# Optimization experiments

Measured on AMD Instinct MI355X. Metric: run time of the kernel, lower is better.

The kernel has to match this reference:

```python
import jax, jax.numpy as jnp
import numpy as np

STRIDES = (8, 16, 32)
SIZES = ((80, 80), (40, 40), (20, 20))  # 640x640 input
PRE_TOP_K = 1000
KEEP_TOP_K = 100
IOU_THR = 0.65
SCORE_THR = 0.25
CLASS_OFFSET = 4096.0  # > max image extent, for class-aware NMS


def setup_inputs() -> dict:
    key = jax.random.key(0)
    ks = jax.random.split(key, 6)
    B, C = 8, 1203
    d = {}
    for i, (h, w) in enumerate(SIZES):
        d[f"cls_scores_{i}"] = jax.random.normal(ks[i], (B, C, h, w), dtype=jnp.float32)
        d[f"bbox_preds_{i}"] = jax.random.uniform(ks[3 + i], (B, 4, h, w), dtype=jnp.float32)
    return d


def _flatten(feats, ch):
    B = feats[0].shape[0]
    return jnp.concatenate([f.transpose(0, 2, 3, 1).reshape(B, -1, ch) for f in feats], axis=1)


def _priors():
    pts, strs = [], []
    for (h, w), s in zip(SIZES, STRIDES):
        yy, xx = jnp.meshgrid(jnp.arange(h, dtype=jnp.float32), jnp.arange(w, dtype=jnp.float32), indexing="ij")
        pts.append(jnp.stack([(xx.ravel() + 0.5) * s, (yy.ravel() + 0.5) * s], axis=-1))
        strs.append(jnp.full((h * w,), float(s), dtype=jnp.float32))
    return jnp.concatenate(pts, 0), jnp.concatenate(strs, 0)


def _decode(priors, preds, stride):
    # DistancePointBBoxCoder: preds are LTRB distances scaled by stride.
    d = preds * stride[None, :, None]  # [B,N,4]
    x1 = priors[None, :, 0] - d[..., 0]
    y1 = priors[None, :, 1] - d[..., 1]
    x2 = priors[None, :, 0] + d[..., 2]
    y2 = priors[None, :, 1] + d[..., 3]
    return jnp.stack([x1, y1, x2, y2], axis=-1)


def _iou_matrix(b):
    area = (b[:, 2] - b[:, 0]) * (b[:, 3] - b[:, 1])
    lt = jnp.maximum(b[:, None, :2], b[None, :, :2])
    rb = jnp.minimum(b[:, None, 2:], b[None, :, 2:])
    wh = jnp.clip(rb - lt, 0.0)
    inter = wh[..., 0] * wh[..., 1]
    return inter / (area[:, None] + area[None, :] - inter + 1e-7)


def _nms_single(boxes, scores, labels):
    # boxes [N,4], scores [N] (max over classes), labels [N] int
    ts, idx = jax.lax.top_k(scores, PRE_TOP_K)
    b = boxes[idx]
    l = labels[idx]
    valid = ts > SCORE_THR
    off = b + (l.astype(b.dtype) * CLASS_OFFSET)[:, None]  # class-aware trick
    iou = _iou_matrix(off)  # [K,K]

    def body(keep, i):
        suppressed = jnp.any(keep & (iou[:, i] > IOU_THR))
        keep = keep.at[i].set(valid[i] & ~suppressed)
        return keep, None

    keep, _ = jax.lax.scan(body, jnp.zeros((PRE_TOP_K,), bool), jnp.arange(PRE_TOP_K))
    kept_scores = jnp.where(keep, ts, -1.0)
    fs, fi = jax.lax.top_k(kept_scores, KEEP_TOP_K)
    m = fs > 0.0
    det_boxes = jnp.where(m[:, None], b[fi], 0.0)
    det_scores = jnp.where(m, fs, 0.0)
    det_labels = jnp.where(m, l[fi], -1)
    num_dets = m.sum().astype(jnp.int32)
    return num_dets, det_boxes, det_scores, det_labels


def reference(cls_scores_0, cls_scores_1, cls_scores_2, bbox_preds_0, bbox_preds_1, bbox_preds_2):
    C = cls_scores_0.shape[1]
    cls_scores = jax.nn.sigmoid(_flatten([cls_scores_0, cls_scores_1, cls_scores_2], C))  # [B,N,C]
    preds = _flatten([bbox_preds_0, bbox_preds_1, bbox_preds_2], 4)  # [B,N,4]
    priors, stride = _priors()
    boxes = _decode(priors, preds, stride)  # [B,N,4]
    max_scores = cls_scores.max(axis=-1)  # [B,N]
    labels = cls_scores.argmax(axis=-1)  # [B,N]
    num_dets, det_boxes, det_scores, det_labels = jax.vmap(_nms_single)(boxes, max_scores, labels)
    return num_dets, det_boxes, det_scores, det_labels
```

## Files before the change

### kernel.cpp

```cpp
#include <hip/hip_runtime.h>
#include <math.h>

#pragma clang fp contract(off)

typedef unsigned long long u64;
typedef unsigned int u32;
typedef float f4 __attribute__((ext_vector_type(4)));
typedef unsigned long long u64x2 __attribute__((ext_vector_type(2)));

#define BB 8
#define CC_TOT 1203
#define NANC 8400
#define NSEL 1000
#define NCAND 1024
#define NT 1024
#define NBATCH 128
#define NCHUNK_MAX 16

__device__ __forceinline__ u32 okey32(float v) {
  u32 b = __float_as_uint(v);
  return (b & 0x80000000u) ? ~b : (b | 0x80000000u);
}

__device__ __forceinline__ float unokey32(u32 ok) {
  u32 fb = (ok & 0x80000000u) ? (ok & 0x7FFFFFFFu) : ~ok;
  return __uint_as_float(fb);
}

__global__ __launch_bounds__(256) void kmax(const float* __restrict__ cls0,
                                            const float* __restrict__ cls1,
                                            const float* __restrict__ cls2,
                                            u64* __restrict__ part,
                                            int chunkSz, int nchunk) {
  int bx = blockIdx.x;
  int per = nchunk * BB;
  int tg = bx / per;
  int rem = bx - tg * per;
  int chunk = rem >> 3;
  int b = rem & 7;
  const float* cls; int hw4, aoff, col0;
  if (tg < 7)      { cls = cls0; hw4 = 1600; aoff = 0;    col0 = tg << 8; }
  else if (tg < 9) { cls = cls1; hw4 = 400;  aoff = 6400; col0 = (tg - 7) << 8; }
  else             { cls = cls2; hw4 = 100;  aoff = 8000; col0 = 0; }
  int col = col0 + (int)threadIdx.x;
  if (col >= hw4) return;
  int c0 = chunk * chunkSz;
  int c1 = c0 + chunkSz; if (c1 > CC_TOT) c1 = CC_TOT;

  const f4* base = (const f4*)cls + (size_t)b * CC_TOT * hw4 + col;
  f4 m = (f4){-3.4e38f, -3.4e38f, -3.4e38f, -3.4e38f};
  int ix0 = c0, ix1 = c0, ix2 = c0, ix3 = c0;

#define UPD(v, c)                                   \
  do {                                              \
    if ((v)[0] > m[0]) { m[0] = (v)[0]; ix0 = (c); } \
    if ((v)[1] > m[1]) { m[1] = (v)[1]; ix1 = (c); } \
    if ((v)[2] > m[2]) { m[2] = (v)[2]; ix2 = (c); } \
    if ((v)[3] > m[3]) { m[3] = (v)[3]; ix3 = (c); } \
  } while (0)

  int c = c0;
  for (; c + 8 <= c1; c += 8) {
    const f4* p = base + (size_t)c * hw4;
    f4 v0 = p[0];
    f4 v1 = p[(size_t)1 * hw4];
    f4 v2 = p[(size_t)2 * hw4];
    f4 v3 = p[(size_t)3 * hw4];
    f4 v4 = p[(size_t)4 * hw4];
    f4 v5 = p[(size_t)5 * hw4];
    f4 v6 = p[(size_t)6 * hw4];
    f4 v7 = p[(size_t)7 * hw4];
    UPD(v0, c + 0); UPD(v1, c + 1); UPD(v2, c + 2); UPD(v3, c + 3);
    UPD(v4, c + 4); UPD(v5, c + 5); UPD(v6, c + 6); UPD(v7, c + 7);
  }
  for (; c < c1; ++c) {
    f4 v = base[(size_t)c * hw4];
    UPD(v, c);
  }
#undef UPD

  u64* dst = part + ((size_t)chunk * BB + b) * NANC + aoff + (size_t)col * 4;
  u64x2 s01 = { ((u64)okey32(m[0]) << 32) | (u64)(u32)~(u32)ix0,
                ((u64)okey32(m[1]) << 32) | (u64)(u32)~(u32)ix1 };
  u64x2 s23 = { ((u64)okey32(m[2]) << 32) | (u64)(u32)~(u32)ix2,
                ((u64)okey32(m[3]) << 32) | (u64)(u32)~(u32)ix3 };
  *((u64x2*)dst)     = s01;
  *((u64x2*)dst + 1) = s23;
}

struct DecodeArrays {
  float xo1[NCAND], yo1[NCAND], xo2[NCAND], yo2[NCAND], ar[NCAND];
  float rx1[NCAND], ry1[NCAND], rx2[NCAND], ry2[NCAND], sc[NCAND];
  int lab[NCAND], val[NCAND];
};

__device__ __forceinline__ u64x2 reduce_pair(const u64x2* psrc, size_t PL2, int nchunk, int i) {
  u64x2 m = psrc[i];
  for (int ch = 1; ch < nchunk; ++ch) {
    u64x2 v = psrc[(size_t)ch * PL2 + i];
    if (v[0] > m[0]) m[0] = v[0];
    if (v[1] > m[1]) m[1] = v[1];
  }
  u32 i0 = (u32)(2 * i), i1 = (u32)(2 * i + 1);
  u64x2 r;
  r[0] = (m[0] & 0xFFFFFFFF00000000ull) | ((u64)(0xFFFFu - i0) << 16) | (u64)(~(u32)m[0] & 0xFFFFu);
  r[1] = (m[1] & 0xFFFFFFFF00000000ull) | ((u64)(0xFFFFu - i1) << 16) | (u64)(~(u32)m[1] & 0xFFFFu);
  return r;
}

__device__ __forceinline__ void hist_add12(u32* hist, u32 digit, int lane) {
  u64 peers = ~0ull;
  for (int bit = 0; bit < 12; ++bit) {
    u64 bal = __ballot((digit >> bit) & 1u);
    peers &= ((digit >> bit) & 1u) ? bal : ~bal;
  }
  int leader = __ffsll((unsigned long long)peers) - 1;
  if (lane == leader)
    atomicAdd(&hist[digit], (u32)__popcll((unsigned long long)peers));
}

__device__ __forceinline__ void hist_add_clustered(u32* hist, u32 digit, int lane) {
  u64 peers = ~0ull;
  for (int bit = 0; bit < 13; ++bit) {
    u64 bal = __ballot((digit >> bit) & 1u);
    peers &= ((digit >> bit) & 1u) ? bal : ~bal;
  }
  int leader = __ffsll((unsigned long long)peers) - 1;
  if (digit < 4096u && lane == leader)
    atomicAdd(&hist[digit], (u32)__popcll((unsigned long long)peers));
}

__device__ __forceinline__ void suffix_pick(u32* hist, u32* waveTot, u32* waveSufExcl,
                                            u64* prefixSh, u32* rankSh, u32* binCntSh,
                                            u64 prefix, u32 rank, int shift,
                                            int tid, int lane, int wv) {
  u32 l0 = hist[4 * tid], l1 = hist[4 * tid + 1], l2 = hist[4 * tid + 2], l3 = hist[4 * tid + 3];
  u32 psum = l0 + l1 + l2 + l3;
  u32 x = psum;
  for (int s = 1; s < 64; s <<= 1) { u32 v = __shfl_down(x, s); if (lane + s < 64) x += v; }
  if (lane == 0) waveTot[wv] = x;
  __syncthreads();
  if (tid < 16) {
    u32 y = waveTot[tid]; u32 z = y;
    for (int s = 1; s < 16; s <<= 1) { u32 v = __shfl_down(z, s); if (tid + s < 16) z += v; }
    waveSufExcl[tid] = z - y;
  }
  __syncthreads();
  u32 S = x + waveSufExcl[wv];
  u32 G3 = S - psum; u32 G2 = G3 + l3; u32 G1 = G2 + l2; u32 G0 = G1 + l1;
  u32 r = rank;
  if      (G3 < r && G3 + l3 >= r) { *prefixSh = prefix | ((u64)(4u * tid + 3) << shift); *rankSh = r - G3; *binCntSh = l3; }
  else if (G2 < r && G2 + l2 >= r) { *prefixSh = prefix | ((u64)(4u * tid + 2) << shift); *rankSh = r - G2; *binCntSh = l2; }
  else if (G1 < r && G1 + l1 >= r) { *prefixSh = prefix | ((u64)(4u * tid + 1) << shift); *rankSh = r - G1; *binCntSh = l1; }
  else if (G0 < r && G0 + l0 >= r) { *prefixSh = prefix | ((u64)(4u * tid + 0) << shift); *rankSh = r - G0; *binCntSh = l0; }
}

__device__ __forceinline__ u64 radix_select(const u64* keys, int n, u32 target,
                                            u32* hist, u32* waveTot, u32* waveSufExcl,
                                            u64* prefixSh, u32* rankSh, u32* binCntSh,
                                            int tid, int lane, int wv) {
  u64 prefix = 0; u32 rank = target;
  for (int pass = 3; pass >= 0; --pass) {
    int shift = 16 + pass * 12;
    for (int i = tid; i < 4096; i += NT) hist[i] = 0;
    __syncthreads();
    u64 hiMask = (pass == 3) ? 0ull : ((~0ull) << (shift + 12));
    if (pass == 3) {
      for (int i = tid; i < n; i += NT) {
        u64 k = keys[i];
        hist_add_clustered(hist, (u32)((k >> shift) & 4095u), lane);
      }
    } else {
      for (int i = tid; i < n; i += NT) {
        u64 k = keys[i];
        if ((k & hiMask) == (prefix & hiMask))
          atomicAdd(&hist[(u32)((k >> shift) & 4095u)], 1u);
      }
    }
    __syncthreads();
    suffix_pick(hist, waveTot, waveSufExcl, prefixSh, rankSh, binCntSh, prefix, rank, shift, tid, lane, wv);
    __syncthreads();
    prefix = *prefixSh; rank = *rankSh;
    __syncthreads();
  }
  return prefix;
}

__device__ __forceinline__ void gather_ge(const u64* keys, int n, u64 K, u64* dst, u32* cnt,
                                          int tid, int lane, u32 bound) {
  for (int i = tid; i < n; i += NT) {
    u64 k = keys[i];
    bool sel = (k >= K);
    u64 mask = __ballot(sel);
    if (mask) {
      int leader = __ffsll((unsigned long long)mask) - 1;
      u32 basep = 0;
      if (lane == leader) basep = atomicAdd(cnt, (u32)__popcll((unsigned long long)mask));
      basep = __shfl((int)basep, leader);
      if (sel) {
        u32 pos = basep + (u32)__popcll((unsigned long long)(mask & ((1ull << lane) - 1ull)));
        if (pos < bound) dst[pos] = k;
      }
    }
  }
}

__device__ __forceinline__ void decode_into(DecodeArrays* d, int rk, u64 my, int b,
                                            const float* bb0, const float* bb1, const float* bb2) {
  int label = (int)(u32)(my & 0xFFFFull);
  int idx = 0xFFFF - (int)(u32)((my >> 16) & 0xFFFFull);
  float logit = unokey32((u32)(my >> 32));
  float sc = 1.0f / (1.0f + expf(-logit));

  int w, str, off, hwl; const float* bb;
  if (idx < 6400)      { w = 80; str = 8;  off = 0;    hwl = 6400; bb = bb0; }
  else if (idx < 8000) { w = 40; str = 16; off = 6400; hwl = 1600; bb = bb1; }
  else                 { w = 20; str = 32; off = 8000; hwl = 400;  bb = bb2; }
  int p = idx - off;
  int y = p / w;
  int x = p - y * w;
  float fs = (float)str;
  float px = ((float)x + 0.5f) * fs;
  float py = ((float)y + 0.5f) * fs;
  const float* bp = bb + (size_t)b * 4 * hwl + p;
  float t0 = bp[0] * fs;
  float t1 = bp[hwl] * fs;
  float t2 = bp[2 * hwl] * fs;
  float t3 = bp[3 * hwl] * fs;
  float x1 = px - t0, y1 = py - t1, x2 = px + t2, y2 = py + t3;
  float lo = (float)label * 4096.0f;
  float ox1 = x1 + lo, oy1 = y1 + lo, ox2 = x2 + lo, oy2 = y2 + lo;
  float area = (ox2 - ox1) * (oy2 - oy1);

  d->xo1[rk] = ox1; d->yo1[rk] = oy1; d->xo2[rk] = ox2; d->yo2[rk] = oy2; d->ar[rk] = area;
  d->rx1[rk] = x1;  d->ry1[rk] = y1;  d->rx2[rk] = x2;  d->ry2[rk] = y2;  d->sc[rk] = sc;
  d->lab[rk] = label;
  d->val[rk] = (sc > 0.25f) ? 1 : 0;
}

__device__ __forceinline__ int nms_pass(const DecodeArrays* d, int bound, int lane, int* outIdx) {
  float ax1 = 0, ay1 = 0, ax2 = 0, ay2 = 0, aar = 0; int aon = 0;
  float bx1 = 0, by1 = 0, bx2 = 0, by2 = 0, bar = 0; int bon = 0;
  int kept = 0;
  for (int i = 0; i < bound; ++i) {
    if (kept >= 100) break;
    float cx1 = d->xo1[i], cy1 = d->yo1[i], cx2 = d->xo2[i], cy2 = d->yo2[i], car = d->ar[i];
    bool sup = false;
    if (aon) {
      float ltx = fmaxf(ax1, cx1), lty = fmaxf(ay1, cy1);
      float rbx = fminf(ax2, cx2), rby = fminf(ay2, cy2);
      float wd = fmaxf(rbx - ltx, 0.0f), ht = fmaxf(rby - lty, 0.0f);
      float inter = wd * ht;
      sup = sup || ((inter / (aar + car - inter + 1e-7f)) > 0.65f);
    }
    if (bon) {
      float ltx = fmaxf(bx1, cx1), lty = fmaxf(by1, cy1);
      float rbx = fminf(bx2, cx2), rby = fminf(by2, cy2);
      float wd = fmaxf(rbx - ltx, 0.0f), ht = fmaxf(rby - lty, 0.0f);
      float inter = wd * ht;
      sup = sup || ((inter / (bar + car - inter + 1e-7f)) > 0.65f);
    }
    bool anysup = __any(sup);
    if (d->val[i] != 0 && !anysup) {
      if (kept < 64) {
        if (lane == kept) { ax1 = cx1; ay1 = cy1; ax2 = cx2; ay2 = cy2; aar = car; aon = 1; }
      } else {
        if (lane == kept - 64) { bx1 = cx1; by1 = cy1; bx2 = cx2; by2 = cy2; bar = car; bon = 1; }
      }
      if (lane == 0) outIdx[kept] = i;
      ++kept;
    }
  }
  return kept;
}

__global__ __launch_bounds__(1024) void knms(const u64* __restrict__ part, int nchunk,
                                             const float* __restrict__ bb0,
                                             const float* __restrict__ bb1,
                                             const float* __restrict__ bb2,
                                             float* __restrict__ out) {
  __shared__ union ShU {
    u64 fk[NANC];
    DecodeArrays d;
  } sh;
  __shared__ u32 hist[4096];
  __shared__ u32 waveTot[16];
  __shared__ u32 waveSufExcl[16];
  __shared__ u64 prefixSh;
  __shared__ u32 rankSh, binCntSh;
  __shared__ u32 gcnt, aCnt, cCnt;
  __shared__ __align__(16) u64 cand[NCAND];
  __shared__ __align__(16) u64 candA[NBATCH];
  __shared__ __align__(16) u32 cm[NBATCH * 4];
  __shared__ u64 VwSh[2];
  __shared__ int outIdx[128];
  __shared__ int keptSh;

  int b = blockIdx.x;
  int tid = threadIdx.x;
  int lane = tid & 63;
  int wv = tid >> 6;

  const u64x2* psrc = (const u64x2*)(part + (size_t)b * NANC);
  const size_t PL2 = (size_t)BB * NANC / 2;

  for (int i = tid; i < 4096; i += NT) hist[i] = 0;
  if (tid == 0) { aCnt = 0; cCnt = 0; }
  __syncthreads();
  {
    u64x2* fdst = (u64x2*)sh.fk;
    for (int i = tid; i < NANC / 2; i += NT) {
      u64x2 k = reduce_pair(psrc, PL2, nchunk, i);
      fdst[i] = k;
      hist_add12(hist, (u32)(k[0] >> 52), lane);
      hist_add12(hist, (u32)(k[1] >> 52), lane);
    }
  }
  __syncthreads();

  suffix_pick(hist, waveTot, waveSufExcl, &prefixSh, &rankSh, &binCntSh,
              0ull, NBATCH, 52, tid, lane, wv);
  __syncthreads();
  u64 pfx3 = prefixSh; u32 r3 = rankSh; u32 l3 = binCntSh;
  u32 d3 = (u32)(pfx3 >> 52);
  __syncthreads();

  bool pathological = false;
  if (l3 == r3) {
    gather_ge(sh.fk, NANC, pfx3, candA, &aCnt, tid, lane, NBATCH);
    __syncthreads();
  } else {
    for (int i = tid; i < NANC; i += NT) {
      u64 k = sh.fk[i];
      u32 dig = (u32)(k >> 52);
      bool selA = dig > d3;
      u64 mA = __ballot(selA);
      if (mA) {
        int leader = __ffsll((unsigned long long)mA) - 1;
        u32 basep = 0;
        if (lane == leader) basep = atomicAdd(&aCnt, (u32)__popcll((unsigned long long)mA));
        basep = __shfl((int)basep, leader);
        if (selA) {
          u32 pos = basep + (u32)__popcll((unsigned long long)(mA & ((1ull << lane) - 1ull)));
          if (pos < NBATCH) candA[pos] = k;
        }
      }
      bool selC = (dig == d3);
      u64 mC = __ballot(selC);
      if (mC) {
        int leader = __ffsll((unsigned long long)mC) - 1;
        u32 basep = 0;
        if (lane == leader) basep = atomicAdd(&cCnt, (u32)__popcll((unsigned long long)mC));
        basep = __shfl((int)basep, leader);
        if (selC) {
          u32 pos = basep + (u32)__popcll((unsigned long long)(mC & ((1ull << lane) - 1ull)));
          if (pos < NCAND) cand[pos] = k;
        }
      }
    }
    __syncthreads();

    u32 cnt3 = cCnt;
    if (cnt3 <= NCAND) {
      u64 pfx = pfx3; u32 rk = r3;
      u64 Kf = 0; bool done = false;
      for (int pass = 2; pass >= 0 && !done; --pass) {
        int shift = 16 + pass * 12;
        for (int i = tid; i < 4096; i += NT) hist[i] = 0;
        __syncthreads();
        u64 hiMask = (~0ull) << (shift + 12);
        for (int i = tid; i < (int)cnt3; i += NT) {
          u64 k = cand[i];
          if ((k & hiMask) == (pfx & hiMask))
            atomicAdd(&hist[(u32)((k >> shift) & 4095u)], 1u);
        }
        __syncthreads();
        suffix_pick(hist, waveTot, waveSufExcl, &prefixSh, &rankSh, &binCntSh,
                    pfx, rk, shift, tid, lane, wv);
        __syncthreads();
        pfx = prefixSh; rk = rankSh;
        u32 lc = binCntSh;
        __syncthreads();
        if (lc == rk || pass == 0) { done = true; Kf = pfx; }
      }
      gather_ge(cand, (int)cnt3, Kf, candA, &aCnt, tid, lane, NBATCH);
      __syncthreads();
    } else {
      pathological = true;
    }
  }

  if (pathological) {
    if (tid == 0) aCnt = 0;
    __syncthreads();
    u64 K2 = radix_select(sh.fk, NANC, NBATCH, hist, waveTot, waveSufExcl,
                          &prefixSh, &rankSh, &binCntSh, tid, lane, wv);
    gather_ge(sh.fk, NANC, K2, candA, &aCnt, tid, lane, NBATCH);
    __syncthreads();
  }

  if (tid < NBATCH) {
    u64 my = candA[tid];
    int rk = 0;
    const u64x2* cav = (const u64x2*)candA;
    #pragma unroll
    for (int j2 = 0; j2 < NBATCH / 2; ++j2) {
      u64x2 p = cav[j2];
      rk += (p[0] > my) ? 1 : 0;
      rk += (p[1] > my) ? 1 : 0;
    }
    decode_into(&sh.d, rk, my, b, bb0, bb1, bb2);
  }
  if (tid < NBATCH * 4) cm[tid] = 0;
  __syncthreads();

  if (tid < NBATCH) {
    u64 bal = __ballot(sh.d.val[tid] != 0);
    if (lane == 0) VwSh[tid >> 6] = bal;
  }

  {
    int c = tid & 127;
    int g = tid >> 7;
    float cx1 = sh.d.xo1[c], cy1 = sh.d.yo1[c], cx2 = sh.d.xo2[c], cy2 = sh.d.yo2[c], car = sh.d.ar[c];
    u32 bits = 0;
    int j0 = g * 16;
    for (int jj = 0; jj < 16; ++jj) {
      int j = j0 + jj;
      float ltx = fmaxf(sh.d.xo1[j], cx1), lty = fmaxf(sh.d.yo1[j], cy1);
      float rbx = fminf(sh.d.xo2[j], cx2), rby = fminf(sh.d.yo2[j], cy2);
      float wd = fmaxf(rbx - ltx, 0.0f), ht = fmaxf(rby - lty, 0.0f);
      float inter = wd * ht;
      bool sup = (inter / (sh.d.ar[j] + car - inter + 1e-7f)) > 0.65f;
      bits |= sup ? (1u << jj) : 0u;
    }
    atomicOr(&cm[c * 4 + (g >> 1)], bits << ((g & 1) * 16));
  }
  __syncthreads();

  if (tid == 0) {
    u32 L0 = (u32)VwSh[0], L1 = (u32)(VwSh[0] >> 32);
    u32 L2 = (u32)VwSh[1], L3 = (u32)(VwSh[1] >> 32);
    int kept = 0;
    while (kept < 100) {
      int i;
      if (L0)      i = __ffs(L0) - 1;
      else if (L1) i = 31 + __ffs(L1);
      else if (L2) i = 63 + __ffs(L2);
      else if (L3) i = 95 + __ffs(L3);
      else break;
      outIdx[kept++] = i;
      const u32* c4 = &cm[i * 4];
      L0 &= ~c4[0]; L1 &= ~c4[1]; L2 &= ~c4[2]; L3 &= ~c4[3];
      if (i < 32)      L0 &= ~(1u << i);
      else if (i < 64) L1 &= ~(1u << (i - 32));
      else if (i < 96) L2 &= ~(1u << (i - 64));
      else             L3 &= ~(1u << (i - 96));
    }
    keptSh = kept;
  }
  __syncthreads();

  if (keptSh < 100) {
    {
      u64x2* fdst = (u64x2*)sh.fk;
      for (int i = tid; i < NANC / 2; i += NT)
        fdst[i] = reduce_pair(psrc, PL2, nchunk, i);
    }
    __syncthreads();
    u64 K = radix_select(sh.fk, NANC, NSEL, hist, waveTot, waveSufExcl,
                         &prefixSh, &rankSh, &binCntSh, tid, lane, wv);
    if (tid == 0) gcnt = 0;
    __syncthreads();
    gather_ge(sh.fk, NANC, K, cand, &gcnt, tid, lane, NSEL);
    __syncthreads();
    if (tid < NSEL) {
      u64 my = cand[tid];
      int rk = 0;
      const u64x2* cbv = (const u64x2*)cand;
      for (int j2 = 0; j2 < NSEL / 2; ++j2) {
        u64x2 p = cbv[j2];
        rk += (p[0] > my) ? 1 : 0;
        rk += (p[1] > my) ? 1 : 0;
      }
      decode_into(&sh.d, rk, my, b, bb0, bb1, bb2);
    }
    __syncthreads();
    if (tid < 64) {
      int kept = nms_pass(&sh.d, NSEL, lane, outIdx);
      if (lane == 0) keptSh = kept;
    }
    __syncthreads();
  }

  int kept = keptSh;
  float* o_nd = out;
  float* o_box = out + BB;
  float* o_sc = out + BB + BB * 100 * 4;
  float* o_lb = out + BB + BB * 100 * 4 + BB * 100;
  if (tid == 0) o_nd[b] = (float)kept;
  if (tid < 100) {
    int s = tid;
    float v0 = 0, v1 = 0, v2 = 0, v3 = 0, sv = 0, lv = -1.0f;
    if (s < kept) {
      int i = outIdx[s];
      v0 = sh.d.rx1[i]; v1 = sh.d.ry1[i]; v2 = sh.d.rx2[i]; v3 = sh.d.ry2[i];
      sv = sh.d.sc[i]; lv = (float)sh.d.lab[i];
    }
    float* bo = o_box + ((size_t)b * 100 + s) * 4;
    bo[0] = v0; bo[1] = v1; bo[2] = v2; bo[3] = v3;
    o_sc[b * 100 + s] = sv;
    o_lb[b * 100 + s] = lv;
  }
}

extern "C" void kernel_launch(void* const* d_in, const int* in_sizes, int n_in,
                              void* d_out, int out_size, void* d_ws, size_t ws_size,
                              hipStream_t stream) {
  const float* cls0 = (const float*)d_in[0];
  const float* bb0  = (const float*)d_in[1];
  const float* cls1 = (const float*)d_in[2];
  const float* bb1  = (const float*)d_in[3];
  const float* cls2 = (const float*)d_in[4];
  const float* bb2  = (const float*)d_in[5];

  size_t planeB = (size_t)BB * NANC * sizeof(u64);
  u64* part = (u64*)d_ws;
  int nchunk = (int)(ws_size / planeB);
  if (nchunk < 1) nchunk = 1;
  if (nchunk > NCHUNK_MAX) nchunk = NCHUNK_MAX;
  int chunkSz = (CC_TOT + nchunk - 1) / nchunk;
  nchunk = (CC_TOT + chunkSz - 1) / chunkSz;

  kmax<<<dim3(10 * nchunk * BB), dim3(256), 0, stream>>>(cls0, cls1, cls2, part, chunkSz, nchunk);
  knms<<<dim3(BB), dim3(NT), 0, stream>>>(part, nchunk, bb0, bb1, bb2, (float*)d_out);
}
```

Before: 132.6 us.

## Split top-k selection into per-segment kernel plus merge kernel

Adds a kernel that splits each image's 8400 anchors into 8 segments. Each of 64 blocks reduces the chunk maxima for its segment and radix-selects the local top 128. The final kernel then selects the global top 128 from only 1024 candidates, so the serial per-batch chunk reduction and histogram work no longer runs on just 8 blocks. It also adds an early exit to the radix select and costs one extra launch plus a global round trip for the candidates.

Measured after the change: 119.8 us. 1.11x faster.

```diff
diff --git a/kernel.cpp b/kernel.cpp
--- a/kernel.cpp
+++ b/kernel.cpp
@@ -11,6 +11,8 @@
 #define BB 8
 #define CC_TOT 1203
 #define NANC 8400
+#define NSEG 8
+#define SEGN 1050
 #define NSEL 1000
 #define NCAND 1024
 #define NT 1024
@@ -94,32 +96,7 @@
   int lab[NCAND], val[NCAND];
 };
 
-__device__ __forceinline__ u64x2 reduce_pair(const u64x2* psrc, size_t PL2, int nchunk, int i) {
-  u64x2 m = psrc[i];
-  for (int ch = 1; ch < nchunk; ++ch) {
-    u64x2 v = psrc[(size_t)ch * PL2 + i];
-    if (v[0] > m[0]) m[0] = v[0];
-    if (v[1] > m[1]) m[1] = v[1];
-  }
-  u32 i0 = (u32)(2 * i), i1 = (u32)(2 * i + 1);
-  u64x2 r;
-  r[0] = (m[0] & 0xFFFFFFFF00000000ull) | ((u64)(0xFFFFu - i0) << 16) | (u64)(~(u32)m[0] & 0xFFFFu);
-  r[1] = (m[1] & 0xFFFFFFFF00000000ull) | ((u64)(0xFFFFu - i1) << 16) | (u64)(~(u32)m[1] & 0xFFFFu);
-  return r;
-}
-
-__device__ __forceinline__ void hist_add12(u32* hist, u32 digit, int lane) {
-  u64 peers = ~0ull;
-  for (int bit = 0; bit < 12; ++bit) {
-    u64 bal = __ballot((digit >> bit) & 1u);
-    peers &= ((digit >> bit) & 1u) ? bal : ~bal;
-  }
-  int leader = __ffsll((unsigned long long)peers) - 1;
-  if (lane == leader)
-    atomicAdd(&hist[digit], (u32)__popcll((unsigned long long)peers));
-}
-
-__device__ __forceinline__ void hist_add_clustered(u32* hist, u32 digit, int lane) {
+__device__ __forceinline__ void hist_addc(u32* hist, u32 digit, int lane) {
   u64 peers = ~0ull;
   for (int bit = 0; bit < 13; ++bit) {
     u64 bal = __ballot((digit >> bit) & 1u);
@@ -155,35 +132,35 @@
   else if (G0 < r && G0 + l0 >= r) { *prefixSh = prefix | ((u64)(4u * tid + 0) << shift); *rankSh = r - G0; *binCntSh = l0; }
 }
 
-__device__ __forceinline__ u64 radix_select(const u64* keys, int n, u32 target,
-                                            u32* hist, u32* waveTot, u32* waveSufExcl,
-                                            u64* prefixSh, u32* rankSh, u32* binCntSh,
-                                            int tid, int lane, int wv) {
-  u64 prefix = 0; u32 rank = target;
-  for (int pass = 3; pass >= 0; --pass) {
+__device__ __forceinline__ u64 select_after_hist(const u64* keys, int n, u32 target,
+                                                 u32* hist, u32* waveTot, u32* waveSufExcl,
+                                                 u64* prefixSh, u32* rankSh, u32* binCntSh,
+                                                 int tid, int lane, int wv) {
+  suffix_pick(hist, waveTot, waveSufExcl, prefixSh, rankSh, binCntSh,
+              0ull, target, 52, tid, lane, wv);
+  __syncthreads();
+  u64 pfx = *prefixSh; u32 rk = *rankSh; u32 lc = *binCntSh;
+  __syncthreads();
+  if (lc == rk) return pfx;
+  for (int pass = 2; pass >= 0; --pass) {
     int shift = 16 + pass * 12;
     for (int i = tid; i < 4096; i += NT) hist[i] = 0;
     __syncthreads();
-    u64 hiMask = (pass == 3) ? 0ull : ((~0ull) << (shift + 12));
-    if (pass == 3) {
-      for (int i = tid; i < n; i += NT) {
-        u64 k = keys[i];
-        hist_add_clustered(hist, (u32)((k >> shift) & 4095u), lane);
-      }
-    } else {
-      for (int i = tid; i < n; i += NT) {
-        u64 k = keys[i];
-        if ((k & hiMask) == (prefix & hiMask))
-          atomicAdd(&hist[(u32)((k >> shift) & 4095u)], 1u);
-      }
-    }
-    __syncthreads();
-    suffix_pick(hist, waveTot, waveSufExcl, prefixSh, rankSh, binCntSh, prefix, rank, shift, tid, lane, wv);
-    __syncthreads();
-    prefix = *prefixSh; rank = *rankSh;
-    __syncthreads();
-  }
-  return prefix;
+    u64 hiMask = (~0ull) << (shift + 12);
+    for (int i = tid; i < n; i += NT) {
+      u64 k = keys[i];
+      if ((k & hiMask) == (pfx & hiMask))
+        atomicAdd(&hist[(u32)((k >> shift) & 4095u)], 1u);
+    }
+    __syncthreads();
+    suffix_pick(hist, waveTot, waveSufExcl, prefixSh, rankSh, binCntSh,
+                pfx, rk, shift, tid, lane, wv);
+    __syncthreads();
+    pfx = *prefixSh; rk = *rankSh; lc = *binCntSh;
+    __syncthreads();
+    if (lc == rk) break;
+  }
+  return pfx;
 }
 
 __device__ __forceinline__ void gather_ge(const u64* keys, int n, u64 K, u64* dst, u32* cnt,
@@ -203,6 +180,69 @@
       }
     }
   }
+}
+
+__global__ __launch_bounds__(1024) void kseg(const u64* __restrict__ part, int nchunk,
+                                             u64* __restrict__ candSeg) {
+  __shared__ __align__(16) u64 keys[SEGN];
+  __shared__ u32 hist[4096];
+  __shared__ u32 waveTot[16], waveSufExcl[16];
+  __shared__ u64 prefixSh;
+  __shared__ u32 rankSh, binCntSh, cnt;
+
+  int seg = blockIdx.x >> 3;
+  int b = blockIdx.x & 7;
+  int tid = threadIdx.x, lane = tid & 63, wv = tid >> 6;
+  int a0 = seg * SEGN;
+
+  const u64x2* psrc = (const u64x2*)part + ((size_t)b * NANC + a0) / 2;
+  const size_t PL2 = (size_t)BB * NANC / 2;
+
+  for (int i = tid; i < 4096; i += NT) hist[i] = 0;
+  if (tid == 0) cnt = 0;
+  __syncthreads();
+
+  {
+    u32 d0 = 4096u, d1 = 4096u;
+    if (tid < SEGN / 2) {
+      u64x2 m = psrc[tid];
+      int ch = 1;
+      for (; ch + 4 <= nchunk; ch += 4) {
+        u64x2 v0 = psrc[(size_t)(ch + 0) * PL2 + tid];
+        u64x2 v1 = psrc[(size_t)(ch + 1) * PL2 + tid];
+        u64x2 v2 = psrc[(size_t)(ch + 2) * PL2 + tid];
+        u64x2 v3 = psrc[(size_t)(ch + 3) * PL2 + tid];
+        u64 a01 = (v0[0] > v1[0]) ? v0[0] : v1[0];
+        u64 a23 = (v2[0] > v3[0]) ? v2[0] : v3[0];
+        u64 aa = (a01 > a23) ? a01 : a23;
+        if (aa > m[0]) m[0] = aa;
+        u64 b01 = (v0[1] > v1[1]) ? v0[1] : v1[1];
+        u64 b23 = (v2[1] > v3[1]) ? v2[1] : v3[1];
+        u64 bb2_ = (b01 > b23) ? b01 : b23;
+        if (bb2_ > m[1]) m[1] = bb2_;
+      }
+      for (; ch < nchunk; ++ch) {
+        u64x2 v = psrc[(size_t)ch * PL2 + tid];
+        if (v[0] > m[0]) m[0] = v[0];
+        if (v[1] > m[1]) m[1] = v[1];
+      }
+      u32 aA = (u32)(a0 + 2 * tid), aB = aA + 1;
+      u64 k0 = (m[0] & 0xFFFFFFFF00000000ull) | ((u64)(0xFFFFu - aA) << 16) | (u64)(~(u32)m[0] & 0xFFFFu);
+      u64 k1 = (m[1] & 0xFFFFFFFF00000000ull) | ((u64)(0xFFFFu - aB) << 16) | (u64)(~(u32)m[1] & 0xFFFFu);
+      keys[2 * tid] = k0;
+      keys[2 * tid + 1] = k1;
+      d0 = (u32)(k0 >> 52);
+      d1 = (u32)(k1 >> 52);
+    }
+    hist_addc(hist, d0, lane);
+    hist_addc(hist, d1, lane);
+  }
+  __syncthreads();
+
+  u64 K = select_after_hist(keys, SEGN, NBATCH, hist, waveTot, waveSufExcl,
+                            &prefixSh, &rankSh, &binCntSh, tid, lane, wv);
+  gather_ge(keys, SEGN, K, candSeg + ((size_t)b * NSEG + seg) * NBATCH, &cnt,
+            tid, lane, NBATCH);
 }
 
 __device__ __forceinline__ void decode_into(DecodeArrays* d, int rk, u64 my, int b,
@@ -274,21 +314,21 @@
   return kept;
 }
 
-__global__ __launch_bounds__(1024) void knms(const u64* __restrict__ part, int nchunk,
-                                             const float* __restrict__ bb0,
-                                             const float* __restrict__ bb1,
-                                             const float* __restrict__ bb2,
-                                             float* __restrict__ out) {
+__global__ __launch_bounds__(1024) void kmerge(const u64* __restrict__ part, int nchunk,
+                                               const u64* __restrict__ candSeg,
+                                               const float* __restrict__ bb0,
+                                               const float* __restrict__ bb1,
+                                               const float* __restrict__ bb2,
+                                               float* __restrict__ out) {
   __shared__ union ShU {
     u64 fk[NANC];
     DecodeArrays d;
   } sh;
   __shared__ u32 hist[4096];
-  __shared__ u32 waveTot[16];
-  __shared__ u32 waveSufExcl[16];
+  __shared__ u32 waveTot[16], waveSufExcl[16];
   __shared__ u64 prefixSh;
   __shared__ u32 rankSh, binCntSh;
-  __shared__ u32 gcnt, aCnt, cCnt;
+  __shared__ u32 gcnt, aCnt;
   __shared__ __align__(16) u64 cand[NCAND];
   __shared__ __align__(16) u64 candA[NBATCH];
   __shared__ __align__(16) u32 cm[NBATCH * 4];
@@ -301,103 +341,19 @@
   int lane = tid & 63;
   int wv = tid >> 6;
 
-  const u64x2* psrc = (const u64x2*)(part + (size_t)b * NANC);
-  const size_t PL2 = (size_t)BB * NANC / 2;
-
   for (int i = tid; i < 4096; i += NT) hist[i] = 0;
-  if (tid == 0) { aCnt = 0; cCnt = 0; }
-  __syncthreads();
-  {
-    u64x2* fdst = (u64x2*)sh.fk;
-    for (int i = tid; i < NANC / 2; i += NT) {
-      u64x2 k = reduce_pair(psrc, PL2, nchunk, i);
-      fdst[i] = k;
-      hist_add12(hist, (u32)(k[0] >> 52), lane);
-      hist_add12(hist, (u32)(k[1] >> 52), lane);
-    }
-  }
-  __syncthreads();
-
-  suffix_pick(hist, waveTot, waveSufExcl, &prefixSh, &rankSh, &binCntSh,
-              0ull, NBATCH, 52, tid, lane, wv);
-  __syncthreads();
-  u64 pfx3 = prefixSh; u32 r3 = rankSh; u32 l3 = binCntSh;
-  u32 d3 = (u32)(pfx3 >> 52);
-  __syncthreads();
-
-  bool pathological = false;
-  if (l3 == r3) {
-    gather_ge(sh.fk, NANC, pfx3, candA, &aCnt, tid, lane, NBATCH);
-    __syncthreads();
-  } else {
-    for (int i = tid; i < NANC; i += NT) {
-      u64 k = sh.fk[i];
-      u32 dig = (u32)(k >> 52);
-      bool selA = dig > d3;
-      u64 mA = __ballot(selA);
-      if (mA) {
-        int leader = __ffsll((unsigned long long)mA) - 1;
-        u32 basep = 0;
-        if (lane == leader) basep = atomicAdd(&aCnt, (u32)__popcll((unsigned long long)mA));
-        basep = __shfl((int)basep, leader);
-        if (selA) {
-          u32 pos = basep + (u32)__popcll((unsigned long long)(mA & ((1ull << lane) - 1ull)));
-          if (pos < NBATCH) candA[pos] = k;
-        }
-      }
-      bool selC = (dig == d3);
-      u64 mC = __ballot(selC);
-      if (mC) {
-        int leader = __ffsll((unsigned long long)mC) - 1;
-        u32 basep = 0;
-        if (lane == leader) basep = atomicAdd(&cCnt, (u32)__popcll((unsigned long long)mC));
-        basep = __shfl((int)basep, leader);
-        if (selC) {
-          u32 pos = basep + (u32)__popcll((unsigned long long)(mC & ((1ull << lane) - 1ull)));
-          if (pos < NCAND) cand[pos] = k;
-        }
-      }
-    }
-    __syncthreads();
-
-    u32 cnt3 = cCnt;
-    if (cnt3 <= NCAND) {
-      u64 pfx = pfx3; u32 rk = r3;
-      u64 Kf = 0; bool done = false;
-      for (int pass = 2; pass >= 0 && !done; --pass) {
-        int shift = 16 + pass * 12;
-        for (int i = tid; i < 4096; i += NT) hist[i] = 0;
-        __syncthreads();
-        u64 hiMask = (~0ull) << (shift + 12);
-        for (int i = tid; i < (int)cnt3; i += NT) {
-          u64 k = cand[i];
-          if ((k & hiMask) == (pfx & hiMask))
-            atomicAdd(&hist[(u32)((k >> shift) & 4095u)], 1u);
-        }
-        __syncthreads();
-        suffix_pick(hist, waveTot, waveSufExcl, &prefixSh, &rankSh, &binCntSh,
-                    pfx, rk, shift, tid, lane, wv);
-        __syncthreads();
-        pfx = prefixSh; rk = rankSh;
-        u32 lc = binCntSh;
-        __syncthreads();
-        if (lc == rk || pass == 0) { done = true; Kf = pfx; }
-      }
-      gather_ge(cand, (int)cnt3, Kf, candA, &aCnt, tid, lane, NBATCH);
-      __syncthreads();
-    } else {
-      pathological = true;
-    }
-  }
-
-  if (pathological) {
-    if (tid == 0) aCnt = 0;
-    __syncthreads();
-    u64 K2 = radix_select(sh.fk, NANC, NBATCH, hist, waveTot, waveSufExcl,
-                          &prefixSh, &rankSh, &binCntSh, tid, lane, wv);
-    gather_ge(sh.fk, NANC, K2, candA, &aCnt, tid, lane, NBATCH);
-    __syncthreads();
-  }
+  if (tid == 0) { gcnt = 0; aCnt = 0; }
+  __syncthreads();
+  u64 myk = candSeg[(size_t)b * (NSEG * NBATCH) + tid];
+  cand[tid] = myk;
+  hist_addc(hist, (u32)(myk >> 52), lane);
+  if (tid < NBATCH * 4) cm[tid] = 0;
+  __syncthreads();
+
+  u64 K = select_after_hist(cand, NCAND, NBATCH, hist, waveTot, waveSufExcl,
+                            &prefixSh, &rankSh, &binCntSh, tid, lane, wv);
+  gather_ge(cand, NCAND, K, candA, &aCnt, tid, lane, NBATCH);
+  __syncthreads();
 
   if (tid < NBATCH) {
     u64 my = candA[tid];
@@ -411,7 +367,6 @@
     }
     decode_into(&sh.d, rk, my, b, bb0, bb1, bb2);
   }
-  if (tid < NBATCH * 4) cm[tid] = 0;
   __syncthreads();
 
   if (tid < NBATCH) {
@@ -462,17 +417,32 @@
   __syncthreads();
 
   if (keptSh < 100) {
+    const u64x2* psrc = (const u64x2*)(part + (size_t)b * NANC);
+    const size_t PL2 = (size_t)BB * NANC / 2;
+    for (int i = tid; i < 4096; i += NT) hist[i] = 0;
+    __syncthreads();
     {
       u64x2* fdst = (u64x2*)sh.fk;
-      for (int i = tid; i < NANC / 2; i += NT)
-        fdst[i] = reduce_pair(psrc, PL2, nchunk, i);
-    }
-    __syncthreads();
-    u64 K = radix_select(sh.fk, NANC, NSEL, hist, waveTot, waveSufExcl,
-                         &prefixSh, &rankSh, &binCntSh, tid, lane, wv);
-    if (tid == 0) gcnt = 0;
-    __syncthreads();
-    gather_ge(sh.fk, NANC, K, cand, &gcnt, tid, lane, NSEL);
+      for (int i = tid; i < NANC / 2; i += NT) {
+        u64x2 m = psrc[i];
+        for (int ch = 1; ch < nchunk; ++ch) {
+          u64x2 v = psrc[(size_t)ch * PL2 + i];
+          if (v[0] > m[0]) m[0] = v[0];
+          if (v[1] > m[1]) m[1] = v[1];
+        }
+        u32 i0 = (u32)(2 * i), i1 = (u32)(2 * i + 1);
+        u64x2 r;
+        r[0] = (m[0] & 0xFFFFFFFF00000000ull) | ((u64)(0xFFFFu - i0) << 16) | (u64)(~(u32)m[0] & 0xFFFFu);
+        r[1] = (m[1] & 0xFFFFFFFF00000000ull) | ((u64)(0xFFFFu - i1) << 16) | (u64)(~(u32)m[1] & 0xFFFFu);
+        fdst[i] = r;
+        hist_addc(hist, (u32)(r[0] >> 52), lane);
+        hist_addc(hist, (u32)(r[1] >> 52), lane);
+      }
+    }
+    __syncthreads();
+    u64 Kf = select_after_hist(sh.fk, NANC, NSEL, hist, waveTot, waveSufExcl,
+                               &prefixSh, &rankSh, &binCntSh, tid, lane, wv);
+    gather_ge(sh.fk, NANC, Kf, cand, &gcnt, tid, lane, NSEL);
     __syncthreads();
     if (tid < NSEL) {
       u64 my = cand[tid];
@@ -525,13 +495,19 @@
   const float* bb2  = (const float*)d_in[5];
 
   size_t planeB = (size_t)BB * NANC * sizeof(u64);
+  size_t candB = (size_t)BB * NSEG * NBATCH * sizeof(u64);
   u64* part = (u64*)d_ws;
-  int nchunk = (int)(ws_size / planeB);
-  if (nchunk < 1) nchunk = 1;
-  if (nchunk > NCHUNK_MAX) nchunk = NCHUNK_MAX;
+  int nchunk = 1;
+  if (ws_size > candB + planeB) {
+    nchunk = (int)((ws_size - candB) / planeB);
+    if (nchunk > NCHUNK_MAX) nchunk = NCHUNK_MAX;
+    if (nchunk < 1) nchunk = 1;
+  }
   int chunkSz = (CC_TOT + nchunk - 1) / nchunk;
   nchunk = (CC_TOT + chunkSz - 1) / chunkSz;
+  u64* candSeg = part + (size_t)nchunk * BB * NANC;
 
   kmax<<<dim3(10 * nchunk * BB), dim3(256), 0, stream>>>(cls0, cls1, cls2, part, chunkSz, nchunk);
-  knms<<<dim3(BB), dim3(NT), 0, stream>>>(part, nchunk, bb0, bb1, bb2, (float*)d_out);
-}
+  kseg<<<dim3(NSEG * BB), dim3(NT), 0, stream>>>(part, nchunk, candSeg);
+  kmerge<<<dim3(BB), dim3(NT), 0, stream>>>(part, nchunk, candSeg, bb0, bb1, bb2, (float*)d_out);
+}
```
